# Kernel optimization log

Hardware: AMD Instinct MI355X
Metric: run time of the kernel (lower is better)

The kernel has to match this reference:

```python
import jax, jax.numpy as jnp
import numpy as np

N_NODES = 50000
N_EDGES = 800000
IN_FEATS = 128
SAGE_HID = 512
H_FEATS = 128
MLP_HID = 32
N_PARTS = 8


def setup_inputs() -> dict:
    key = jax.random.key(0)
    ks = jax.random.split(key, 16)
    s = 0.05
    return {
        "features": jax.random.normal(ks[0], (N_NODES, IN_FEATS), jnp.float32),
        "src": jax.random.randint(ks[1], (N_EDGES,), 0, N_NODES),
        "dst": jax.random.randint(ks[2], (N_EDGES,), 0, N_NODES),
        # SAGEConv layer 1 (in_feats -> 512): fc_self has bias, fc_neigh no bias
        "W1_self": jax.random.normal(ks[3], (IN_FEATS, SAGE_HID), jnp.float32) * s,
        "W1_neigh": jax.random.normal(ks[4], (IN_FEATS, SAGE_HID), jnp.float32) * s,
        "b1": jnp.zeros((SAGE_HID,), jnp.float32),
        # SAGEConv layer 2 (512 -> h_feats)
        "W2_self": jax.random.normal(ks[5], (SAGE_HID, H_FEATS), jnp.float32) * s,
        "W2_neigh": jax.random.normal(ks[6], (SAGE_HID, H_FEATS), jnp.float32) * s,
        "b2": jnp.zeros((H_FEATS,), jnp.float32),
        # Partitioning MLP
        "Wp1": jax.random.normal(ks[7], (H_FEATS, MLP_HID), jnp.float32) * s,
        "bp1": jnp.zeros((MLP_HID,), jnp.float32),
        "Wp2": jax.random.normal(ks[8], (MLP_HID, N_PARTS), jnp.float32) * s,
        "bp2": jnp.zeros((N_PARTS,), jnp.float32),
    }


def _sage_mean(x, src, dst, deg_inv, W_self, W_neigh, b):
    # gather source-node features per edge, sum by destination, divide by in-degree
    agg = jax.ops.segment_sum(jnp.take(x, src, axis=0), dst, num_segments=N_NODES)
    agg = agg * deg_inv[:, None]
    return x @ W_self + agg @ W_neigh + b


def reference(features, src, dst, W1_self, W1_neigh, b1, W2_self, W2_neigh, b2,
              Wp1, bp1, Wp2, bp2):
    deg = jax.ops.segment_sum(jnp.ones_like(dst, dtype=features.dtype), dst,
                              num_segments=N_NODES)
    deg_inv = 1.0 / jnp.maximum(deg, 1.0)
    h = jax.nn.relu(_sage_mean(features, src, dst, deg_inv, W1_self, W1_neigh, b1))
    h = jax.nn.relu(_sage_mean(h, src, dst, deg_inv, W2_self, W2_neigh, b2))
    x = jax.nn.relu(h @ Wp1 + bp1)
    logits = x @ Wp2 + bp2
    return jax.nn.softmax(logits, axis=1)
```

## Files before the change

kernel.cpp:

```cpp
#include <hip/hip_runtime.h>
#include <hip/hip_bf16.h>

#define N_NODES 50000
#define N_EDGES 800000

typedef short  short8  __attribute__((ext_vector_type(8)));
typedef float  floatx4 __attribute__((ext_vector_type(4)));

__device__ __forceinline__ short f2bf(float f) {
    union { __hip_bfloat16 h; short s; } u;
    u.h = __float2bfloat16(f);
    return u.s;
}
__device__ __forceinline__ float2 upk(unsigned v) {
    union { float f; unsigned u; } a, b;
    a.u = v << 16; b.u = v & 0xffff0000u;
    return make_float2(a.f, b.f);
}
__device__ __forceinline__ unsigned packbf(float lo, float hi) {
    return ((unsigned)(unsigned short)f2bf(hi) << 16) | (unsigned short)f2bf(lo);
}

__device__ __forceinline__ void gld_lds16(const short* g, short* l) {
    __builtin_amdgcn_global_load_lds(
        (const __attribute__((address_space(1))) int*)g,
        (__attribute__((address_space(3))) int*)l, 16, 0, 0);
}

__global__ void k_deg(const int* __restrict__ dst, int* __restrict__ deg) {
    int e = blockIdx.x * 256 + threadIdx.x;
    if (e < N_EDGES) atomicAdd(&deg[dst[e]], 1);
}

__global__ __launch_bounds__(1024) void k_scan1(const int* __restrict__ deg,
                                                int* __restrict__ bsum,
                                                float* __restrict__ dinv) {
    __shared__ int ws[16];
    int b = blockIdx.x, t = threadIdx.x, i = b * 1024 + t;
    int lane = t & 63, wid = t >> 6;
    int v = (i < N_NODES) ? deg[i] : 0;
    if (i < N_NODES) dinv[i] = 1.0f / fmaxf((float)v, 1.0f);
    int x = v;
    #pragma unroll
    for (int off = 1; off < 64; off <<= 1) x += __shfl_xor(x, off, 64);
    if (lane == 0) ws[wid] = x;
    __syncthreads();
    if (t == 0) {
        int s = 0;
        #pragma unroll
        for (int k = 0; k < 16; ++k) s += ws[k];
        bsum[b] = s;
    }
}

__global__ void k_scan2(const int* __restrict__ bsum, int* __restrict__ boff) {
    int lane = threadIdx.x;
    int v = (lane < 49) ? bsum[lane] : 0;
    int x = v;
    #pragma unroll
    for (int off = 1; off < 64; off <<= 1) {
        int y = __shfl_up(x, off, 64);
        if (lane >= off) x += y;
    }
    if (lane < 49) boff[lane] = x - v;
}

__global__ __launch_bounds__(1024) void k_scan3(const int* __restrict__ deg,
                                                const int* __restrict__ boff,
                                                int* __restrict__ rowptr,
                                                int* __restrict__ cursor) {
    __shared__ int ws[16];
    int b = blockIdx.x, t = threadIdx.x, i = b * 1024 + t;
    int lane = t & 63, wid = t >> 6;
    int v = (i < N_NODES) ? deg[i] : 0;
    int x = v;
    #pragma unroll
    for (int off = 1; off < 64; off <<= 1) {
        int y = __shfl_up(x, off, 64);
        if (lane >= off) x += y;
    }
    if (lane == 63) ws[wid] = x;
    __syncthreads();
    if (wid == 0) {
        int s = (lane < 16) ? ws[lane] : 0;
        #pragma unroll
        for (int off = 1; off < 16; off <<= 1) {
            int y = __shfl_up(s, off, 64);
            if (lane >= off) s += y;
        }
        if (lane < 16) ws[lane] = s;
    }
    __syncthreads();
    int waveOff = (wid == 0) ? 0 : ws[wid - 1];
    int incl = x + waveOff + boff[b];
    if (i < N_NODES) { rowptr[i + 1] = incl; cursor[i] = incl - v; }
    if (b == 0 && t == 0) rowptr[0] = 0;
}

__global__ void k_fill(const int* __restrict__ src, const int* __restrict__ dst,
                       int* __restrict__ cursor, int* __restrict__ col) {
    int e = blockIdx.x * 256 + threadIdx.x;
    if (e < N_EDGES) {
        int d = dst[e];
        int p = atomicAdd(&cursor[d], 1);
        col[p] = src[e];
    }
}

__global__ void k_cvt(const float* __restrict__ feat,
                      const float* __restrict__ W1s, const float* __restrict__ W1n,
                      const float* __restrict__ W2s, const float* __restrict__ W2n,
                      short* __restrict__ Abf, short* __restrict__ W1T,
                      short* __restrict__ W2T) {
    int bb = blockIdx.x, t = threadIdx.x;
    if (bb < 6250) {
        int idx = bb * 256 + t;
        if (idx >= N_NODES * 32) return;
        int n = idx >> 5, c = (idx & 31) * 4;
        float4 v = *(const float4*)(feat + (size_t)n * 128 + c);
        *(short4*)(Abf + (size_t)n * 256 + c) =
            make_short4(f2bf(v.x), f2bf(v.y), f2bf(v.z), f2bf(v.w));
    } else {
        int idx = (bb - 6250) * 256 + t;
        if (idx < 512 * 256) {
            int n = idx >> 8, k = idx & 255;
            float v = (k < 128) ? W1s[(size_t)k * 512 + n]
                                : W1n[(size_t)(k - 128) * 512 + n];
            W1T[idx] = f2bf(v);
        } else {
            int j = idx - 512 * 256;
            int n = j >> 9, k = j & 511;
            float v = (n < 128) ? W2s[(size_t)k * 128 + n]
                                : W2n[(size_t)k * 128 + (n - 128)];
            W2T[j] = f2bf(v);
        }
    }
}

template<int STRIDE>
__device__ __forceinline__ float2 wave_gather(
    const unsigned* __restrict__ U, const int* __restrict__ col,
    int s, int e, int lane) {
    float ax = 0.f, ay = 0.f;
    for (int base = s; base < e; base += 64) {
        int cnt = e - base; if (cnt > 64) cnt = 64;
        int myc = (base + lane < e) ? col[base + lane] : 0;
        int j = 0;
        for (; j + 16 <= cnt; j += 16) {
            unsigned v[16];
            #pragma unroll
            for (int u = 0; u < 16; ++u) {
                int c = __builtin_amdgcn_readlane(myc, j + u);
                v[u] = U[(size_t)c * STRIDE + lane];
            }
            #pragma unroll
            for (int u = 0; u < 16; ++u) {
                float2 f = upk(v[u]); ax += f.x; ay += f.y;
            }
        }
        for (; j + 8 <= cnt; j += 8) {
            unsigned v[8];
            #pragma unroll
            for (int u = 0; u < 8; ++u) {
                int c = __builtin_amdgcn_readlane(myc, j + u);
                v[u] = U[(size_t)c * STRIDE + lane];
            }
            #pragma unroll
            for (int u = 0; u < 8; ++u) {
                float2 f = upk(v[u]); ax += f.x; ay += f.y;
            }
        }
        if (j < cnt) {
            unsigned v[8];
            int m = cnt - j;
            #pragma unroll
            for (int u = 0; u < 8; ++u) {
                if (u < m) {
                    int c = __builtin_amdgcn_readlane(myc, j + u);
                    v[u] = U[(size_t)c * STRIDE + lane];
                }
            }
            #pragma unroll
            for (int u = 0; u < 8; ++u) {
                if (u < m) { float2 f = upk(v[u]); ax += f.x; ay += f.y; }
            }
        }
    }
    return make_float2(ax, ay);
}

__global__ __launch_bounds__(256) void k_agg(
    const unsigned* __restrict__ Au, const int* __restrict__ rowptr,
    const int* __restrict__ col, const float* __restrict__ dinv,
    unsigned* __restrict__ Aw) {
    int t = threadIdx.x, lane = t & 63, w = t >> 6;
    int n = blockIdx.x * 4 + w;
    int s = rowptr[n], e = rowptr[n + 1];
    float2 a = wave_gather<128>(Au, col, s, e, lane);
    float dv = dinv[n];
    Aw[(size_t)n * 128 + 64 + lane] = packbf(a.x * dv, a.y * dv);
}

__global__ __launch_bounds__(256) void k_aggmlp(
    const unsigned* __restrict__ Yu, const int* __restrict__ rowptr,
    const int* __restrict__ col, const float* __restrict__ dinv,
    const float* __restrict__ z, const float* __restrict__ b2,
    const float* __restrict__ Wp1, const float* __restrict__ bp1,
    const float* __restrict__ Wp2, const float* __restrict__ bp2,
    float* __restrict__ out) {
    __shared__ float h2sh[4][128];
    __shared__ float xsh[4][32];
    int t = threadIdx.x, lane = t & 63, w = t >> 6;
    int n = blockIdx.x * 4 + w;
    int s = rowptr[n], e = rowptr[n + 1];
    float2 a = wave_gather<64>(Yu, col, s, e, lane);
    float dv = dinv[n];
    float2 zv = *(const float2*)(z + (size_t)n * 128 + 2 * lane);
    float2 bb = *(const float2*)(b2 + 2 * lane);
    h2sh[w][2 * lane]     = fmaxf(zv.x + a.x * dv + bb.x, 0.f);
    h2sh[w][2 * lane + 1] = fmaxf(zv.y + a.y * dv + bb.y, 0.f);
    int j = lane & 31, half = lane >> 5;
    float p = 0.f;
    #pragma unroll
    for (int k2 = 0; k2 < 64; ++k2) {
        int k = half * 64 + k2;
        p += h2sh[w][k] * Wp1[k * 32 + j];
    }
    p += __shfl_xor(p, 32, 64);
    if (half == 0) xsh[w][j] = fmaxf(p + bp1[j], 0.f);
    if (lane < 8) {
        float lg = bp2[lane];
        #pragma unroll
        for (int jj = 0; jj < 32; ++jj)
            lg += xsh[w][jj] * Wp2[jj * 8 + lane];
        float mx = lg;
        mx = fmaxf(mx, __shfl_xor(mx, 1, 64));
        mx = fmaxf(mx, __shfl_xor(mx, 2, 64));
        mx = fmaxf(mx, __shfl_xor(mx, 4, 64));
        float ev = expf(lg - mx);
        float sm = ev;
        sm += __shfl_xor(sm, 1, 64);
        sm += __shfl_xor(sm, 2, 64);
        sm += __shfl_xor(sm, 4, 64);
        out[(size_t)n * 8 + lane] = ev / sm;
    }
}

template<int K, int N, bool EPI1>
__global__ __launch_bounds__(256) void k_gemm_mfma(
    const short* __restrict__ A, const short* __restrict__ BT,
    const float* __restrict__ bias, short* __restrict__ Obf,
    float* __restrict__ Of0) {
    __shared__ short smem[2 * 128 * 32];
    short* sA = smem;
    short* sB = smem + 128 * 32;
    short* sOut = smem;
    const int t = threadIdx.x;
    const int lane = t & 63;
    const int w = t >> 6;
    const int mBase = blockIdx.x * 128;
    const int nBase = blockIdx.y * 128;
    const int mOff = (w & 1) * 64;
    const int nOff = (w >> 1) * 64;

    floatx4 zero4 = {0.f, 0.f, 0.f, 0.f};
    floatx4 acc[4][4];
    #pragma unroll
    for (int i = 0; i < 4; ++i)
        #pragma unroll
        for (int j = 0; j < 4; ++j) acc[i][j] = zero4;

    const int rL = lane >> 2;
    const int cg = (((lane & 3) ^ ((lane >> 3) & 3))) * 8;
    const int rA = w * 32 + rL;
    const long gA0 = (long)min(mBase + rA,      N_NODES - 1) * K + cg;
    const long gA1 = (long)min(mBase + rA + 16, N_NODES - 1) * K + cg;
    const long gB0 = (long)(nBase + rA)      * K + cg;
    const long gB1 = (long)(nBase + rA + 16) * K + cg;
    short* lA0 = sA + (w * 32) * 32;
    short* lA1 = sA + (w * 32 + 16) * 32;
    short* lB0 = sB + (w * 32) * 32;
    short* lB1 = sB + (w * 32 + 16) * 32;

    const int fr = lane & 15;
    const int csel = (((lane >> 4) ^ ((lane >> 1) & 3))) * 8;

    for (int kt = 0; kt < K / 32; ++kt) {
        const int k0 = kt * 32;
        __syncthreads();
        gld_lds16(A + gA0 + k0, lA0);
        gld_lds16(A + gA1 + k0, lA1);
        gld_lds16(BT + gB0 + k0, lB0);
        gld_lds16(BT + gB1 + k0, lB1);
        __syncthreads();
        short8 af[4], bf[4];
        #pragma unroll
        for (int i = 0; i < 4; ++i) {
            af[i] = *(const short8*)(sA + (mOff + i * 16 + fr) * 32 + csel);
            bf[i] = *(const short8*)(sB + (nOff + i * 16 + fr) * 32 + csel);
        }
        #pragma unroll
        for (int mi = 0; mi < 4; ++mi)
            #pragma unroll
            for (int ni = 0; ni < 4; ++ni)
                acc[mi][ni] = __builtin_amdgcn_mfma_f32_16x16x32_bf16(
                    af[mi], bf[ni], acc[mi][ni], 0, 0, 0);
    }

    const int cn = lane & 15;
    const int cm = (lane >> 4) * 4;

    if (!EPI1 && nBase < 128) {
        #pragma unroll
        for (int ni = 0; ni < 4; ++ni) {
            const int n = nOff + ni * 16 + cn;
            #pragma unroll
            for (int mi = 0; mi < 4; ++mi) {
                #pragma unroll
                for (int r = 0; r < 4; ++r) {
                    const int m = mBase + mOff + mi * 16 + cm + r;
                    if (m < N_NODES) Of0[(size_t)m * 128 + n] = acc[mi][ni][r];
                }
            }
        }
        return;
    }

    float bv[4];
    #pragma unroll
    for (int ni = 0; ni < 4; ++ni)
        bv[ni] = EPI1 ? bias[nBase + nOff + ni * 16 + cn] : 0.f;
    const int myh = mOff >> 6;
    const int ldc = EPI1 ? N : 128;
    const int cbase = EPI1 ? nBase : 0;
    for (int h = 0; h < 2; ++h) {
        __syncthreads();
        if (myh == h) {
            #pragma unroll
            for (int mi = 0; mi < 4; ++mi)
                #pragma unroll
                for (int ni = 0; ni < 4; ++ni)
                    #pragma unroll
                    for (int r = 0; r < 4; ++r) {
                        int mrow = mi * 16 + cm + r;
                        int nloc = nOff + ni * 16 + cn;
                        float v = acc[mi][ni][r];
                        if (EPI1) v = fmaxf(v + bv[ni], 0.f);
                        sOut[mrow * 128 + nloc] = f2bf(v);
                    }
        }
        __syncthreads();
        int r0 = t >> 2, c0 = (t & 3) * 32;
        int m = mBase + h * 64 + r0;
        if (m < N_NODES) {
            const short* sp = sOut + r0 * 128 + c0;
            short* gp = Obf + (size_t)m * ldc + cbase + c0;
            #pragma unroll
            for (int q = 0; q < 4; ++q)
                *(short8*)(gp + q * 8) = *(const short8*)(sp + q * 8);
        }
    }
}

extern "C" void kernel_launch(void* const* d_in, const int* in_sizes, int n_in,
                              void* d_out, int out_size, void* d_ws, size_t ws_size,
                              hipStream_t stream) {
    const float* feat   = (const float*)d_in[0];
    const int*   src    = (const int*)d_in[1];
    const int*   dst    = (const int*)d_in[2];
    const float* W1s    = (const float*)d_in[3];
    const float* W1n    = (const float*)d_in[4];
    const float* b1     = (const float*)d_in[5];
    const float* W2s    = (const float*)d_in[6];
    const float* W2n    = (const float*)d_in[7];
    const float* b2     = (const float*)d_in[8];
    const float* Wp1    = (const float*)d_in[9];
    const float* bp1    = (const float*)d_in[10];
    const float* Wp2    = (const float*)d_in[11];
    const float* bp2    = (const float*)d_in[12];
    float* out = (float*)d_out;

    char* w = (char*)d_ws;
    size_t off = 0;
    auto alloc = [&](size_t bytes) { char* p = w + off; off += (bytes + 255) & ~(size_t)255; return p; };
    int*   deg    = (int*)alloc(N_NODES * 4);
    int*   rowptr = (int*)alloc((N_NODES + 1) * 4);
    int*   cursor = (int*)alloc(N_NODES * 4);
    int*   col    = (int*)alloc(N_EDGES * 4);
    float* dinv   = (float*)alloc(N_NODES * 4);
    int*   bsum   = (int*)alloc(64 * 4);
    int*   boff   = (int*)alloc(64 * 4);
    short* Abf    = (short*)alloc((size_t)N_NODES * 256 * 2);
    short* W1T    = (short*)alloc((size_t)512 * 256 * 2);
    short* W2T    = (short*)alloc((size_t)256 * 512 * 2);
    short* h1bf   = (short*)alloc((size_t)N_NODES * 512 * 2);
    float* z      = (float*)alloc((size_t)N_NODES * 128 * 4);
    short* y1bf   = (short*)alloc((size_t)N_NODES * 128 * 2);

    hipMemsetAsync(deg, 0, N_NODES * 4, stream);
    k_deg<<<N_EDGES / 256, 256, 0, stream>>>(dst, deg);
    k_scan1<<<49, 1024, 0, stream>>>(deg, bsum, dinv);
    k_scan2<<<1, 64, 0, stream>>>(bsum, boff);
    k_scan3<<<49, 1024, 0, stream>>>(deg, boff, rowptr, cursor);
    k_fill<<<N_EDGES / 256, 256, 0, stream>>>(src, dst, cursor, col);
    k_cvt<<<7274, 256, 0, stream>>>(feat, W1s, W1n, W2s, W2n, Abf, W1T, W2T);
    k_agg<<<N_NODES / 4, 256, 0, stream>>>((const unsigned*)Abf, rowptr, col, dinv, (unsigned*)Abf);
    dim3 g1((N_NODES + 127) / 128, 4);
    k_gemm_mfma<256, 512, true><<<g1, 256, 0, stream>>>(Abf, W1T, b1, h1bf, nullptr);
    dim3 g2((N_NODES + 127) / 128, 2);
    k_gemm_mfma<512, 256, false><<<g2, 256, 0, stream>>>(h1bf, W2T, nullptr, y1bf, z);
    k_aggmlp<<<N_NODES / 4, 256, 0, stream>>>((const unsigned*)y1bf, rowptr, col, dinv, z, b2,
                                              Wp1, bp1, Wp2, bp2, out);
}
```

Before: 337.8 us.

## Widen GEMM block tile to 128x256 so each A tile is reused across more columns

Each MFMA GEMM block now computes a 128x256 output tile instead of 128x128, with each wave holding 64x128 accumulators, and the launch grids are halved in the N dimension. For the second GEMM, a single block produces both the fp32 self-term and the bf16 neighbour-term outputs, and the epilogues are restructured to match. The aim is to load the A operand from global memory fewer times and raise the ratio of MFMA work to loads. In exchange, accumulator registers double, which may lower occupancy or cause spills, and there are half as many blocks.

```diff
diff --git a/kernel.cpp b/kernel.cpp
--- a/kernel.cpp
+++ b/kernel.cpp
@@ -251,7 +251,7 @@
     const short* __restrict__ A, const short* __restrict__ BT,
     const float* __restrict__ bias, short* __restrict__ Obf,
     float* __restrict__ Of0) {
-    __shared__ short smem[2 * 128 * 32];
+    __shared__ short smem[64 * 256];
     short* sA = smem;
     short* sB = smem + 128 * 32;
     short* sOut = smem;
@@ -259,28 +259,32 @@
     const int lane = t & 63;
     const int w = t >> 6;
     const int mBase = blockIdx.x * 128;
-    const int nBase = blockIdx.y * 128;
+    const int nBase = blockIdx.y * 256;
     const int mOff = (w & 1) * 64;
-    const int nOff = (w >> 1) * 64;
+    const int nOff = (w >> 1) * 128;
 
     floatx4 zero4 = {0.f, 0.f, 0.f, 0.f};
-    floatx4 acc[4][4];
+    floatx4 acc[4][8];
     #pragma unroll
     for (int i = 0; i < 4; ++i)
         #pragma unroll
-        for (int j = 0; j < 4; ++j) acc[i][j] = zero4;
+        for (int j = 0; j < 8; ++j) acc[i][j] = zero4;
 
     const int rL = lane >> 2;
     const int cg = (((lane & 3) ^ ((lane >> 3) & 3))) * 8;
     const int rA = w * 32 + rL;
     const long gA0 = (long)min(mBase + rA,      N_NODES - 1) * K + cg;
     const long gA1 = (long)min(mBase + rA + 16, N_NODES - 1) * K + cg;
-    const long gB0 = (long)(nBase + rA)      * K + cg;
-    const long gB1 = (long)(nBase + rA + 16) * K + cg;
+    const long gB0 = (long)(nBase + rA)       * K + cg;
+    const long gB1 = (long)(nBase + rA + 16)  * K + cg;
+    const long gB2 = (long)(nBase + rA + 128) * K + cg;
+    const long gB3 = (long)(nBase + rA + 144) * K + cg;
     short* lA0 = sA + (w * 32) * 32;
     short* lA1 = sA + (w * 32 + 16) * 32;
     short* lB0 = sB + (w * 32) * 32;
     short* lB1 = sB + (w * 32 + 16) * 32;
+    short* lB2 = sB + (w * 32 + 128) * 32;
+    short* lB3 = sB + (w * 32 + 144) * 32;
 
     const int fr = lane & 15;
     const int csel = (((lane >> 4) ^ ((lane >> 1) & 3))) * 8;
@@ -292,17 +296,20 @@
         gld_lds16(A + gA1 + k0, lA1);
         gld_lds16(BT + gB0 + k0, lB0);
         gld_lds16(BT + gB1 + k0, lB1);
+        gld_lds16(BT + gB2 + k0, lB2);
+        gld_lds16(BT + gB3 + k0, lB3);
         __syncthreads();
-        short8 af[4], bf[4];
-        #pragma unroll
-        for (int i = 0; i < 4; ++i) {
+        short8 af[4], bf[8];
+        #pragma unroll
+        for (int i = 0; i < 4; ++i)
             af[i] = *(const short8*)(sA + (mOff + i * 16 + fr) * 32 + csel);
+        #pragma unroll
+        for (int i = 0; i < 8; ++i)
             bf[i] = *(const short8*)(sB + (nOff + i * 16 + fr) * 32 + csel);
-        }
         #pragma unroll
         for (int mi = 0; mi < 4; ++mi)
             #pragma unroll
-            for (int ni = 0; ni < 4; ++ni)
+            for (int ni = 0; ni < 8; ++ni)
                 acc[mi][ni] = __builtin_amdgcn_mfma_f32_16x16x32_bf16(
                     af[mi], bf[ni], acc[mi][ni], 0, 0, 0);
     }
@@ -310,54 +317,71 @@
     const int cn = lane & 15;
     const int cm = (lane >> 4) * 4;
 
-    if (!EPI1 && nBase < 128) {
-        #pragma unroll
-        for (int ni = 0; ni < 4; ++ni) {
-            const int n = nOff + ni * 16 + cn;
-            #pragma unroll
-            for (int mi = 0; mi < 4; ++mi) {
+    if constexpr (!EPI1) {
+        if (nOff == 0) {
+            #pragma unroll
+            for (int ni = 0; ni < 8; ++ni) {
+                const int n = ni * 16 + cn;
                 #pragma unroll
-                for (int r = 0; r < 4; ++r) {
-                    const int m = mBase + mOff + mi * 16 + cm + r;
-                    if (m < N_NODES) Of0[(size_t)m * 128 + n] = acc[mi][ni][r];
-                }
-            }
-        }
-        return;
-    }
-
-    float bv[4];
-    #pragma unroll
-    for (int ni = 0; ni < 4; ++ni)
-        bv[ni] = EPI1 ? bias[nBase + nOff + ni * 16 + cn] : 0.f;
-    const int myh = mOff >> 6;
-    const int ldc = EPI1 ? N : 128;
-    const int cbase = EPI1 ? nBase : 0;
-    for (int h = 0; h < 2; ++h) {
-        __syncthreads();
-        if (myh == h) {
-            #pragma unroll
-            for (int mi = 0; mi < 4; ++mi)
-                #pragma unroll
-                for (int ni = 0; ni < 4; ++ni)
+                for (int mi = 0; mi < 4; ++mi)
                     #pragma unroll
                     for (int r = 0; r < 4; ++r) {
-                        int mrow = mi * 16 + cm + r;
-                        int nloc = nOff + ni * 16 + cn;
-                        float v = acc[mi][ni][r];
-                        if (EPI1) v = fmaxf(v + bv[ni], 0.f);
-                        sOut[mrow * 128 + nloc] = f2bf(v);
+                        const int m = mBase + mOff + mi * 16 + cm + r;
+                        if (m < N_NODES) Of0[(size_t)m * 128 + n] = acc[mi][ni][r];
                     }
-        }
-        __syncthreads();
-        int r0 = t >> 2, c0 = (t & 3) * 32;
-        int m = mBase + h * 64 + r0;
-        if (m < N_NODES) {
-            const short* sp = sOut + r0 * 128 + c0;
-            short* gp = Obf + (size_t)m * ldc + cbase + c0;
-            #pragma unroll
-            for (int q = 0; q < 4; ++q)
-                *(short8*)(gp + q * 8) = *(const short8*)(sp + q * 8);
+            }
+        }
+        for (int h = 0; h < 2; ++h) {
+            __syncthreads();
+            if (nOff == 128 && (w & 1) == h) {
+                #pragma unroll
+                for (int mi = 0; mi < 4; ++mi)
+                    #pragma unroll
+                    for (int ni = 0; ni < 8; ++ni)
+                        #pragma unroll
+                        for (int r = 0; r < 4; ++r)
+                            sOut[(mi * 16 + cm + r) * 128 + ni * 16 + cn] =
+                                f2bf(acc[mi][ni][r]);
+            }
+            __syncthreads();
+            int r0 = t >> 2, c0 = (t & 3) * 32;
+            int m = mBase + h * 64 + r0;
+            if (m < N_NODES) {
+                const short* sp = sOut + r0 * 128 + c0;
+                short* gp = Obf + (size_t)m * 128 + c0;
+                #pragma unroll
+                for (int q = 0; q < 4; ++q)
+                    *(short8*)(gp + q * 8) = *(const short8*)(sp + q * 8);
+            }
+        }
+        return;
+    } else {
+        float bv[8];
+        #pragma unroll
+        for (int ni = 0; ni < 8; ++ni)
+            bv[ni] = bias[nBase + nOff + ni * 16 + cn];
+        for (int h = 0; h < 2; ++h) {
+            __syncthreads();
+            if ((w & 1) == h) {
+                #pragma unroll
+                for (int mi = 0; mi < 4; ++mi)
+                    #pragma unroll
+                    for (int ni = 0; ni < 8; ++ni)
+                        #pragma unroll
+                        for (int r = 0; r < 4; ++r)
+                            sOut[(mi * 16 + cm + r) * 256 + nOff + ni * 16 + cn] =
+                                f2bf(fmaxf(acc[mi][ni][r] + bv[ni], 0.f));
+            }
+            __syncthreads();
+            int r0 = t >> 2, c0 = (t & 3) * 64;
+            int m = mBase + h * 64 + r0;
+            if (m < N_NODES) {
+                const short* sp = sOut + r0 * 256 + c0;
+                short* gp = Obf + (size_t)m * N + nBase + c0;
+                #pragma unroll
+                for (int q = 0; q < 8; ++q)
+                    *(short8*)(gp + q * 8) = *(const short8*)(sp + q * 8);
+            }
         }
     }
 }
@@ -405,9 +429,9 @@
     k_fill<<<N_EDGES / 256, 256, 0, stream>>>(src, dst, cursor, col);
     k_cvt<<<7274, 256, 0, stream>>>(feat, W1s, W1n, W2s, W2n, Abf, W1T, W2T);
     k_agg<<<N_NODES / 4, 256, 0, stream>>>((const unsigned*)Abf, rowptr, col, dinv, (unsigned*)Abf);
-    dim3 g1((N_NODES + 127) / 128, 4);
+    dim3 g1((N_NODES + 127) / 128, 2);
     k_gemm_mfma<256, 512, true><<<g1, 256, 0, stream>>>(Abf, W1T, b1, h1bf, nullptr);
-    dim3 g2((N_NODES + 127) / 128, 2);
+    dim3 g2((N_NODES + 127) / 128, 1);
     k_gemm_mfma<512, 256, false><<<g2, 256, 0, stream>>>(h1bf, W2T, nullptr, y1bf, z);
     k_aggmlp<<<N_NODES / 4, 256, 0, stream>>>((const unsigned*)y1bf, rowptr, col, dinv, z, b2,
                                               Wp1, bp1, Wp2, bp2, out);
```

New measurement: 374.0 us. 10.7% more time.
